# Kernel optimization log

Hardware: AMD Instinct MI355X
Metric: run time of the kernel (lower is better)

Reference implementation:

```python
import jax, jax.numpy as jnp
import numpy as np

B, H, N = 128, 512, 1024

def setup_inputs() -> dict:
    key = jax.random.key(0)
    ks = jax.random.split(key, 9)
    s = 1.0 / np.sqrt(H)
    return {
        "mc_hidden": jax.random.normal(ks[0], (B, H), jnp.float32),
        "sn_hidden": jax.random.normal(ks[1], (B, H, N), jnp.float32),
        "attn_W": jax.random.normal(ks[2], (H, 2 * H), jnp.float32) * s,
        "attn_v": jax.random.normal(ks[3], (H,), jnp.float32) * s,
        "ptr_v": jax.random.normal(ks[4], (H,), jnp.float32) * s,
        "fc1_W": jax.random.normal(ks[5], (H, 2 * H), jnp.float32) * s,
        "fc1_b": jax.random.normal(ks[6], (H,), jnp.float32) * s,
        "fc2_W": jax.random.normal(ks[7], (H, H), jnp.float32) * s,
        "fc2_b": jax.random.normal(ks[8], (H,), jnp.float32) * s,
    }


def reference(mc_hidden, sn_hidden, attn_W, attn_v, ptr_v, fc1_W, fc1_b, fc2_W, fc2_b):
    # ---- Attention (Bahdanau-style additive scoring) ----
    # hidden: (B, 2H, N) = cat(sn_hidden, mc expanded along N) on dim 1
    mc_exp = jnp.broadcast_to(mc_hidden[:, :, None], sn_hidden.shape)  # (B,H,N)
    hidden = jnp.concatenate((sn_hidden, mc_exp), axis=1)              # (B,2H,N)
    # W @ hidden -> (B,H,N); v @ tanh(.) -> (B,N)
    scores = jnp.einsum('h,bhn->bn', attn_v,
                        jnp.tanh(jnp.einsum('hk,bkn->bhn', attn_W, hidden)))
    attns = jax.nn.softmax(scores, axis=-1)                            # (B,N)
    # ---- Context + pointer scoring ----
    context = jnp.einsum('bn,bhn->bh', attns, sn_hidden)               # (B,H)
    x = jnp.concatenate((mc_hidden, context), axis=1)                  # (B,2H)
    out = jax.nn.relu(x @ fc1_W.T + fc1_b)                             # (B,H)
    out = jax.nn.relu(out @ fc2_W.T + fc2_b)                           # (B,H)
    probs = jnp.einsum('h,bhn->bn', ptr_v,
                       jnp.tanh(sn_hidden + out[:, :, None]))          # (B,N)
    return probs
```

## Files before the change

kernel.cpp:

```cpp
#include <hip/hip_runtime.h>
#include <hip/hip_bf16.h>

#define Bn 128
#define Hd 512
#define Nn 1024

typedef __attribute__((ext_vector_type(8))) short short8;
typedef __attribute__((ext_vector_type(4))) float f32x4;

#define GLOAD_LDS16(gptr, lptr)                                                     \
    __builtin_amdgcn_global_load_lds(                                               \
        (const __attribute__((address_space(1))) void*)(gptr),                      \
        (__attribute__((address_space(3))) void*)(lptr), 16, 0, 0)

__device__ __forceinline__ float bf2f(unsigned u) {
    unsigned v = u << 16;
    float f;
    __builtin_memcpy(&f, &v, 4);
    return f;
}

__device__ __forceinline__ unsigned short f2bf(float f) {
    unsigned x;
    __builtin_memcpy(&x, &f, 4);
    unsigned r = x + 0x7fffu + ((x >> 16) & 1u);
    return (unsigned short)(r >> 16);
}

__device__ __forceinline__ unsigned pack_bf2(float a, float b) {
    __hip_bfloat162 h = __float22bfloat162_rn(float2{a, b});
    unsigned u;
    __builtin_memcpy(&u, &h, 4);
    return u;
}

__device__ __forceinline__ float wave_sum(float v) {
    v += __shfl_xor(v, 32);
    v += __shfl_xor(v, 16);
    v += __shfl_xor(v, 8);
    v += __shfl_xor(v, 4);
    v += __shfl_xor(v, 2);
    v += __shfl_xor(v, 1);
    return v;
}

__device__ __forceinline__ float tanh_fast(float x) {
    float e = __expf(2.0f * x);
    return 1.0f - 2.0f * __builtin_amdgcn_rcpf(e + 1.0f);
}

__global__ void convert_W_kernel(const float* __restrict__ attn_W,
                                 unsigned short* __restrict__ Wb) {
    int idx = (blockIdx.x * 256 + threadIdx.x) * 8;
    int h = idx >> 9;
    int k = idx & 511;
    const float* p = attn_W + (size_t)h * 1024 + k;
    float4 v0 = *(const float4*)p;
    float4 v1 = *(const float4*)(p + 4);
    unsigned u[4] = {pack_bf2(v0.x, v0.y), pack_bf2(v0.z, v0.w),
                     pack_bf2(v1.x, v1.y), pack_bf2(v1.z, v1.w)};
    *(uint4*)(Wb + idx) = *(uint4*)u;
}

__global__ void transpose_sn_kernel(const float* __restrict__ sn,
                                    unsigned short* __restrict__ snT) {
    __shared__ unsigned ldsb[32 * 132];
    int bid = blockIdx.x;
    int b = bid >> 6;
    int kt = (bid >> 3) & 7;
    int nt = bid & 7;
    int k0 = kt << 6, n0 = nt << 7;
    int t = threadIdx.x;

    int kp_l = t >> 5;
    int n4 = (t & 31) * 4;
#pragma unroll
    for (int j = 0; j < 4; ++j) {
        int kp = j * 8 + kp_l;
        const float* p0 = sn + ((size_t)(b * Hd + k0 + 2 * kp)) * Nn + n0 + n4;
        float4 f0 = *(const float4*)p0;
        float4 f1 = *(const float4*)(p0 + Nn);
        unsigned u[4];
        u[0] = pack_bf2(f0.x, f1.x);
        u[1] = pack_bf2(f0.y, f1.y);
        u[2] = pack_bf2(f0.z, f1.z);
        u[3] = pack_bf2(f0.w, f1.w);
        *(uint4*)&ldsb[kp * 132 + n4] = *(uint4*)u;
    }
    __syncthreads();

    int c = t & 7;
#pragma unroll
    for (int it = 0; it < 4; ++it) {
        int n = (t >> 3) + it * 32;
        unsigned u[4];
#pragma unroll
        for (int i = 0; i < 4; ++i) u[i] = ldsb[(c * 4 + i) * 132 + n];
        unsigned short* dst = snT + ((size_t)(b * Nn) + n0 + n) * Hd + k0 + c * 8;
        *(uint4*)dst = *(uint4*)u;
    }
}

__global__ void mc_term_kernel(const float* __restrict__ mc,
                               const float* __restrict__ attn_W,
                               float* __restrict__ mc_term) {
    int wg = (blockIdx.x * blockDim.x + threadIdx.x) >> 6;
    int lane = threadIdx.x & 63;
    int b = wg >> 9;
    int h = wg & 511;
    const float* m = mc + b * Hd + lane * 8;
    const float* w = attn_W + (size_t)h * 1024 + 512 + lane * 8;
    float4 m0 = *(const float4*)m, m1 = *(const float4*)(m + 4);
    float4 w0 = *(const float4*)w, w1 = *(const float4*)(w + 4);
    float acc = m0.x * w0.x + m0.y * w0.y + m0.z * w0.z + m0.w * w0.w +
                m1.x * w1.x + m1.y * w1.y + m1.z * w1.z + m1.w * w1.w;
    acc = wave_sum(acc);
    if (lane == 0) mc_term[b * Hd + h] = acc;
}

__global__ __launch_bounds__(256, 2)
void attn_score_kernel(const unsigned short* __restrict__ snT,
                       const unsigned short* __restrict__ Wb,
                       const float* __restrict__ attn_v,
                       const float* __restrict__ mc_term,
                       float* __restrict__ scores) {
    __shared__ __align__(16) unsigned short A_lds[256 * 64];
    __shared__ __align__(16) unsigned short B_lds[128 * 64];
    __shared__ float av_s[256];
    __shared__ float mct_s[256];
    __shared__ float ssum[128];

    const int bid = blockIdx.x;
    const int b = bid >> 4;
    const int mh = (bid >> 3) & 1;
    const int n0 = (bid & 7) << 7;
    const int tid = threadIdx.x;
    const int lane = tid & 63;
    const int wid = tid >> 6;
    const int quad = lane >> 4;
    const int l15 = lane & 15;

    av_s[tid] = attn_v[mh * 256 + tid];
    mct_s[tid] = mc_term[b * Hd + mh * 256 + tid];
    if (tid < 128) ssum[tid] = 0.f;

    f32x4 acc[4][8];
#pragma unroll
    for (int i = 0; i < 4; ++i)
#pragma unroll
        for (int j = 0; j < 8; ++j) {
            f32x4 z = {0.f, 0.f, 0.f, 0.f};
            acc[i][j] = z;
        }

    const int r8 = lane >> 3;
    const int csw = ((lane & 7) ^ r8) * 16;
    const char* Wg = (const char*)Wb + (size_t)(mh * 256) * 1024;
    const char* Bg = (const char*)snT + ((size_t)(b * Nn + n0)) * 1024;
    const int key = l15 & 7;

    for (int k0 = 0; k0 < 512; k0 += 64) {
#pragma unroll
        for (int i = 0; i < 8; ++i) {
            const int row = wid * 64 + i * 8;
            GLOAD_LDS16(Wg + (size_t)(row + r8) * 1024 + k0 * 2 + csw,
                        (char*)A_lds + row * 128);
        }
#pragma unroll
        for (int i = 0; i < 4; ++i) {
            const int row = wid * 32 + i * 8;
            GLOAD_LDS16(Bg + (size_t)(row + r8) * 1024 + k0 * 2 + csw,
                        (char*)B_lds + row * 128);
        }
        __syncthreads();
#pragma unroll
        for (int kk = 0; kk < 2; ++kk) {
            const int cb = quad + kk * 4;
            short8 bfr[8], afr[4];
#pragma unroll
            for (int nt = 0; nt < 8; ++nt) {
                const int n = nt * 16 + l15;
                bfr[nt] = *(const short8*)((const char*)B_lds + n * 128 + ((cb ^ key) * 16));
            }
#pragma unroll
            for (int mt = 0; mt < 4; ++mt) {
                const int m = wid * 64 + mt * 16 + l15;
                afr[mt] = *(const short8*)((const char*)A_lds + m * 128 + ((cb ^ key) * 16));
            }
#pragma unroll
            for (int mt = 0; mt < 4; ++mt)
#pragma unroll
                for (int nt = 0; nt < 8; ++nt)
                    acc[mt][nt] = __builtin_amdgcn_mfma_f32_16x16x32_bf16(afr[mt], bfr[nt], acc[mt][nt], 0, 0, 0);
        }
        __syncthreads();
    }

    float s[8] = {0.f, 0.f, 0.f, 0.f, 0.f, 0.f, 0.f, 0.f};
#pragma unroll
    for (int mt = 0; mt < 4; ++mt) {
        int hb = wid * 64 + mt * 16 + quad * 4;
#pragma unroll
        for (int r = 0; r < 4; ++r) {
            float av = av_s[hb + r];
            float mcv = mct_s[hb + r];
#pragma unroll
            for (int nt = 0; nt < 8; ++nt)
                s[nt] += av * tanh_fast(acc[mt][nt][r] + mcv);
        }
    }
#pragma unroll
    for (int nt = 0; nt < 8; ++nt) {
        float v = s[nt];
        v += __shfl_xor(v, 16);
        v += __shfl_xor(v, 32);
        if (lane < 16) atomicAdd(&ssum[nt * 16 + l15], v);
    }
    __syncthreads();
    if (tid < 128) atomicAdd(&scores[b * Nn + n0 + tid], ssum[tid]);
}

__global__ void softmax_context_kernel(const unsigned short* __restrict__ snT,
                                       const float* __restrict__ scores,
                                       float* __restrict__ context) {
    int b = blockIdx.x >> 3;
    int nc = (blockIdx.x & 7) << 7;
    int t = threadIdx.x;
    int lane = t & 63, wid = t >> 6;
    __shared__ float red[4];
    __shared__ float a_s[128];

    float v[4];
#pragma unroll
    for (int i = 0; i < 4; ++i) v[i] = scores[b * Nn + t + i * 256];
    float m = fmaxf(fmaxf(v[0], v[1]), fmaxf(v[2], v[3]));
#pragma unroll
    for (int off = 32; off >= 1; off >>= 1) m = fmaxf(m, __shfl_xor(m, off));
    if (lane == 0) red[wid] = m;
    __syncthreads();
    m = fmaxf(fmaxf(red[0], red[1]), fmaxf(red[2], red[3]));
    __syncthreads();
    float s = 0.f;
#pragma unroll
    for (int i = 0; i < 4; ++i) s += __expf(v[i] - m);
    s = wave_sum(s);
    if (lane == 0) red[wid] = s;
    __syncthreads();
    s = red[0] + red[1] + red[2] + red[3];
    float inv = __builtin_amdgcn_rcpf(s);
    if (t < 128) a_s[t] = __expf(scores[b * Nn + nc + t] - m) * inv;
    __syncthreads();

    const unsigned short* base = snT + ((size_t)(b * Nn) + nc) * Hd + t * 2;
    float acc0 = 0.f, acc1 = 0.f;
#pragma unroll 4
    for (int i = 0; i < 128; ++i) {
        unsigned d = *(const unsigned*)(base + (size_t)i * Hd);
        float a = a_s[i];
        acc0 += a * bf2f(d & 0xffffu);
        acc1 += a * bf2f(d >> 16);
    }
    atomicAdd(&context[b * Hd + 2 * t], acc0);
    atomicAdd(&context[b * Hd + 2 * t + 1], acc1);
}

__global__ void fc1_kernel(const float* __restrict__ mc,
                           const float* __restrict__ ctx,
                           const float* __restrict__ fc1_W,
                           const float* __restrict__ fc1_b,
                           float* __restrict__ out1) {
    int wg = (blockIdx.x * blockDim.x + threadIdx.x) >> 6;
    int lane = threadIdx.x & 63;
    int b = wg >> 9, h = wg & 511;
    const float* wr = fc1_W + (size_t)h * 1024;
    float acc = 0.f;
    {
        float4 w0 = *(const float4*)(wr + lane * 8);
        float4 w1 = *(const float4*)(wr + lane * 8 + 4);
        float4 x0 = *(const float4*)(mc + b * Hd + lane * 8);
        float4 x1 = *(const float4*)(mc + b * Hd + lane * 8 + 4);
        acc += w0.x * x0.x + w0.y * x0.y + w0.z * x0.z + w0.w * x0.w;
        acc += w1.x * x1.x + w1.y * x1.y + w1.z * x1.z + w1.w * x1.w;
    }
    {
        float4 w0 = *(const float4*)(wr + 512 + lane * 8);
        float4 w1 = *(const float4*)(wr + 512 + lane * 8 + 4);
        float4 x0 = *(const float4*)(ctx + b * Hd + lane * 8);
        float4 x1 = *(const float4*)(ctx + b * Hd + lane * 8 + 4);
        acc += w0.x * x0.x + w0.y * x0.y + w0.z * x0.z + w0.w * x0.w;
        acc += w1.x * x1.x + w1.y * x1.y + w1.z * x1.z + w1.w * x1.w;
    }
    acc = wave_sum(acc);
    if (lane == 0) out1[b * Hd + h] = fmaxf(acc + fc1_b[h], 0.f);
}

__global__ void fc2_kernel(const float* __restrict__ out1,
                           const float* __restrict__ fc2_W,
                           const float* __restrict__ fc2_b,
                           float* __restrict__ out2) {
    int wg = (blockIdx.x * blockDim.x + threadIdx.x) >> 6;
    int lane = threadIdx.x & 63;
    int b = wg >> 9, h = wg & 511;
    const float* wr = fc2_W + (size_t)h * 512 + lane * 8;
    float4 w0 = *(const float4*)wr;
    float4 w1 = *(const float4*)(wr + 4);
    float4 x0 = *(const float4*)(out1 + b * Hd + lane * 8);
    float4 x1 = *(const float4*)(out1 + b * Hd + lane * 8 + 4);
    float acc = w0.x * x0.x + w0.y * x0.y + w0.z * x0.z + w0.w * x0.w +
                w1.x * x1.x + w1.y * x1.y + w1.z * x1.z + w1.w * x1.w;
    acc = wave_sum(acc);
    if (lane == 0) out2[b * Hd + h] = fmaxf(acc + fc2_b[h], 0.f);
}

__global__ void final_kernel(const unsigned short* __restrict__ snT,
                             const float* __restrict__ ptr_v,
                             const float* __restrict__ out2,
                             float* __restrict__ probs) {
    int b = blockIdx.x >> 4;
    int n0 = (blockIdx.x & 15) << 6;
    int t = threadIdx.x;
    int n = n0 + (t >> 2), p = t & 3;
    __shared__ float pv_s[512], o2_s[512];
    pv_s[t] = ptr_v[t];
    pv_s[t + 256] = ptr_v[t + 256];
    o2_s[t] = out2[b * Hd + t];
    o2_s[t + 256] = out2[b * Hd + t + 256];
    __syncthreads();
    const unsigned short* row = snT + ((size_t)(b * Nn) + n) * Hd + p * 8;
    float a = 0.f;
#pragma unroll 4
    for (int j = 0; j < 16; ++j) {
        uint4 d = *(const uint4*)(row + j * 32);
        int hb = p * 8 + j * 32;
        const unsigned* u = (const unsigned*)&d;
#pragma unroll
        for (int q = 0; q < 4; ++q) {
            int h = hb + q * 2;
            float x0 = bf2f(u[q] & 0xffffu);
            float x1 = bf2f(u[q] >> 16);
            a += pv_s[h] * tanh_fast(x0 + o2_s[h]);
            a += pv_s[h + 1] * tanh_fast(x1 + o2_s[h + 1]);
        }
    }
    a += __shfl_xor(a, 1);
    a += __shfl_xor(a, 2);
    if (p == 0) probs[b * Nn + n] = a;
}

extern "C" void kernel_launch(void* const* d_in, const int* in_sizes, int n_in,
                              void* d_out, int out_size, void* d_ws, size_t ws_size,
                              hipStream_t stream) {
    const float* mc  = (const float*)d_in[0];
    const float* sn  = (const float*)d_in[1];
    const float* aW  = (const float*)d_in[2];
    const float* av  = (const float*)d_in[3];
    const float* pv  = (const float*)d_in[4];
    const float* f1W = (const float*)d_in[5];
    const float* f1b = (const float*)d_in[6];
    const float* f2W = (const float*)d_in[7];
    const float* f2b = (const float*)d_in[8];

    unsigned short* snT = (unsigned short*)d_ws;
    unsigned short* Wb  = snT + (size_t)Bn * Nn * Hd;
    float* fws     = (float*)(Wb + 512 * 512);
    float* mc_term = fws;
    float* scores  = mc_term + Bn * Hd;
    float* context = scores + Bn * Nn;
    float* out1    = context + Bn * Hd;
    float* out2    = out1 + Bn * Hd;
    float* probs   = (float*)d_out;

    hipMemsetAsync(scores, 0, (Bn * Nn + Bn * Hd) * sizeof(float), stream);
    convert_W_kernel<<<dim3(128), dim3(256), 0, stream>>>(aW, Wb);
    transpose_sn_kernel<<<dim3(8192), dim3(256), 0, stream>>>(sn, snT);
    mc_term_kernel<<<dim3(16384), dim3(256), 0, stream>>>(mc, aW, mc_term);
    attn_score_kernel<<<dim3(2048), dim3(256), 0, stream>>>(snT, Wb, av, mc_term, scores);
    softmax_context_kernel<<<dim3(1024), dim3(256), 0, stream>>>(snT, scores, context);
    fc1_kernel<<<dim3(16384), dim3(256), 0, stream>>>(mc, context, f1W, f1b, out1);
    fc2_kernel<<<dim3(16384), dim3(256), 0, stream>>>(out1, f2W, f2b, out2);
    final_kernel<<<dim3(2048), dim3(256), 0, stream>>>(snT, pv, out2, probs);
}
```

Baseline: 552.7 us.

## Drop sn transpose pass; consume fp32 sn directly in attention, context, final

Removes the separate bf16 transpose of sn_hidden and converts to bf16 on the fly inside the attention MFMA kernel, staging through registers into a k-pair LDS layout. Context and final kernels now read fp32 sn in its native layout with coalesced float4 loads. Softmax is split out, and score atomics are replaced by per-half partial buffers, which removes the memset. The trade is more fp32 bytes read per consumer, with scalar LDS gathers for the B fragments, in exchange for skipping the transpose write and one launch.

```diff
diff --git a/kernel.cpp b/kernel.cpp
--- a/kernel.cpp
+++ b/kernel.cpp
@@ -12,20 +12,6 @@
     __builtin_amdgcn_global_load_lds(                                               \
         (const __attribute__((address_space(1))) void*)(gptr),                      \
         (__attribute__((address_space(3))) void*)(lptr), 16, 0, 0)
-
-__device__ __forceinline__ float bf2f(unsigned u) {
-    unsigned v = u << 16;
-    float f;
-    __builtin_memcpy(&f, &v, 4);
-    return f;
-}
-
-__device__ __forceinline__ unsigned short f2bf(float f) {
-    unsigned x;
-    __builtin_memcpy(&x, &f, 4);
-    unsigned r = x + 0x7fffu + ((x >> 16) & 1u);
-    return (unsigned short)(r >> 16);
-}
 
 __device__ __forceinline__ unsigned pack_bf2(float a, float b) {
     __hip_bfloat162 h = __float22bfloat162_rn(float2{a, b});
@@ -49,62 +35,23 @@
     return 1.0f - 2.0f * __builtin_amdgcn_rcpf(e + 1.0f);
 }
 
-__global__ void convert_W_kernel(const float* __restrict__ attn_W,
-                                 unsigned short* __restrict__ Wb) {
-    int idx = (blockIdx.x * 256 + threadIdx.x) * 8;
-    int h = idx >> 9;
-    int k = idx & 511;
-    const float* p = attn_W + (size_t)h * 1024 + k;
-    float4 v0 = *(const float4*)p;
-    float4 v1 = *(const float4*)(p + 4);
-    unsigned u[4] = {pack_bf2(v0.x, v0.y), pack_bf2(v0.z, v0.w),
-                     pack_bf2(v1.x, v1.y), pack_bf2(v1.z, v1.w)};
-    *(uint4*)(Wb + idx) = *(uint4*)u;
-}
-
-__global__ void transpose_sn_kernel(const float* __restrict__ sn,
-                                    unsigned short* __restrict__ snT) {
-    __shared__ unsigned ldsb[32 * 132];
-    int bid = blockIdx.x;
-    int b = bid >> 6;
-    int kt = (bid >> 3) & 7;
-    int nt = bid & 7;
-    int k0 = kt << 6, n0 = nt << 7;
-    int t = threadIdx.x;
-
-    int kp_l = t >> 5;
-    int n4 = (t & 31) * 4;
-#pragma unroll
-    for (int j = 0; j < 4; ++j) {
-        int kp = j * 8 + kp_l;
-        const float* p0 = sn + ((size_t)(b * Hd + k0 + 2 * kp)) * Nn + n0 + n4;
-        float4 f0 = *(const float4*)p0;
-        float4 f1 = *(const float4*)(p0 + Nn);
-        unsigned u[4];
-        u[0] = pack_bf2(f0.x, f1.x);
-        u[1] = pack_bf2(f0.y, f1.y);
-        u[2] = pack_bf2(f0.z, f1.z);
-        u[3] = pack_bf2(f0.w, f1.w);
-        *(uint4*)&ldsb[kp * 132 + n4] = *(uint4*)u;
-    }
-    __syncthreads();
-
-    int c = t & 7;
-#pragma unroll
-    for (int it = 0; it < 4; ++it) {
-        int n = (t >> 3) + it * 32;
-        unsigned u[4];
-#pragma unroll
-        for (int i = 0; i < 4; ++i) u[i] = ldsb[(c * 4 + i) * 132 + n];
-        unsigned short* dst = snT + ((size_t)(b * Nn) + n0 + n) * Hd + k0 + c * 8;
-        *(uint4*)dst = *(uint4*)u;
-    }
-}
-
-__global__ void mc_term_kernel(const float* __restrict__ mc,
-                               const float* __restrict__ attn_W,
-                               float* __restrict__ mc_term) {
-    int wg = (blockIdx.x * blockDim.x + threadIdx.x) >> 6;
+__global__ void pre_kernel(const float* __restrict__ attn_W,
+                           const float* __restrict__ mc,
+                           unsigned short* __restrict__ Wb,
+                           float* __restrict__ mc_term) {
+    if (blockIdx.x < 128) {
+        int idx = (blockIdx.x * 256 + threadIdx.x) * 8;
+        int h = idx >> 9;
+        int k = idx & 511;
+        const float* p = attn_W + (size_t)h * 1024 + k;
+        float4 v0 = *(const float4*)p;
+        float4 v1 = *(const float4*)(p + 4);
+        unsigned u[4] = {pack_bf2(v0.x, v0.y), pack_bf2(v0.z, v0.w),
+                         pack_bf2(v1.x, v1.y), pack_bf2(v1.z, v1.w)};
+        *(uint4*)(Wb + idx) = *(uint4*)u;
+        return;
+    }
+    int wg = ((blockIdx.x - 128) * 256 + threadIdx.x) >> 6;
     int lane = threadIdx.x & 63;
     int b = wg >> 9;
     int h = wg & 511;
@@ -119,13 +66,13 @@
 }
 
 __global__ __launch_bounds__(256, 2)
-void attn_score_kernel(const unsigned short* __restrict__ snT,
+void attn_score_kernel(const float* __restrict__ sn,
                        const unsigned short* __restrict__ Wb,
                        const float* __restrict__ attn_v,
                        const float* __restrict__ mc_term,
-                       float* __restrict__ scores) {
+                       float* __restrict__ scores_part) {
     __shared__ __align__(16) unsigned short A_lds[256 * 64];
-    __shared__ __align__(16) unsigned short B_lds[128 * 64];
+    __shared__ __align__(16) unsigned B_kp[32 * 132];
     __shared__ float av_s[256];
     __shared__ float mct_s[256];
     __shared__ float ssum[128];
@@ -156,8 +103,11 @@
     const int r8 = lane >> 3;
     const int csw = ((lane & 7) ^ r8) * 16;
     const char* Wg = (const char*)Wb + (size_t)(mh * 256) * 1024;
-    const char* Bg = (const char*)snT + ((size_t)(b * Nn + n0)) * 1024;
     const int key = l15 & 7;
+
+    const int kp_l = tid >> 5;
+    const int n4 = (tid & 31) * 4;
+    const float* snb = sn + (size_t)b * Hd * Nn + n0 + n4;
 
     for (int k0 = 0; k0 < 512; k0 += 64) {
 #pragma unroll
@@ -167,10 +117,17 @@
                         (char*)A_lds + row * 128);
         }
 #pragma unroll
-        for (int i = 0; i < 4; ++i) {
-            const int row = wid * 32 + i * 8;
-            GLOAD_LDS16(Bg + (size_t)(row + r8) * 1024 + k0 * 2 + csw,
-                        (char*)B_lds + row * 128);
+        for (int j = 0; j < 4; ++j) {
+            const int kp = j * 8 + kp_l;
+            const float* p0 = snb + (size_t)(k0 + 2 * kp) * Nn;
+            float4 f0 = *(const float4*)p0;
+            float4 f1 = *(const float4*)(p0 + Nn);
+            unsigned u[4];
+            u[0] = pack_bf2(f0.x, f1.x);
+            u[1] = pack_bf2(f0.y, f1.y);
+            u[2] = pack_bf2(f0.z, f1.z);
+            u[3] = pack_bf2(f0.w, f1.w);
+            *(uint4*)&B_kp[kp * 132 + n4] = *(uint4*)u;
         }
         __syncthreads();
 #pragma unroll
@@ -179,8 +136,13 @@
             short8 bfr[8], afr[4];
 #pragma unroll
             for (int nt = 0; nt < 8; ++nt) {
-                const int n = nt * 16 + l15;
-                bfr[nt] = *(const short8*)((const char*)B_lds + n * 128 + ((cb ^ key) * 16));
+                const int nl = nt * 16 + l15;
+                uint4 uu;
+                uu.x = B_kp[(cb * 4 + 0) * 132 + nl];
+                uu.y = B_kp[(cb * 4 + 1) * 132 + nl];
+                uu.z = B_kp[(cb * 4 + 2) * 132 + nl];
+                uu.w = B_kp[(cb * 4 + 3) * 132 + nl];
+                bfr[nt] = *(short8*)&uu;
             }
 #pragma unroll
             for (int mt = 0; mt < 4; ++mt) {
@@ -217,22 +179,24 @@
         if (lane < 16) atomicAdd(&ssum[nt * 16 + l15], v);
     }
     __syncthreads();
-    if (tid < 128) atomicAdd(&scores[b * Nn + n0 + tid], ssum[tid]);
-}
-
-__global__ void softmax_context_kernel(const unsigned short* __restrict__ snT,
-                                       const float* __restrict__ scores,
-                                       float* __restrict__ context) {
-    int b = blockIdx.x >> 3;
-    int nc = (blockIdx.x & 7) << 7;
-    int t = threadIdx.x;
-    int lane = t & 63, wid = t >> 6;
+    if (tid < 128)
+        scores_part[((size_t)mh * Bn + b) * Nn + n0 + tid] = ssum[tid];
+}
+
+__global__ void softmax_kernel(const float* __restrict__ scores_part,
+                               float* __restrict__ attns) {
+    const int b = blockIdx.x;
+    const int tid = threadIdx.x;
+    const int lane = tid & 63, wid = tid >> 6;
     __shared__ float red[4];
-    __shared__ float a_s[128];
-
+    const float* s0 = scores_part + (size_t)b * Nn;
+    const float* s1 = scores_part + ((size_t)Bn + b) * Nn;
     float v[4];
 #pragma unroll
-    for (int i = 0; i < 4; ++i) v[i] = scores[b * Nn + t + i * 256];
+    for (int i = 0; i < 4; ++i) {
+        int idx = tid + i * 256;
+        v[i] = s0[idx] + s1[idx];
+    }
     float m = fmaxf(fmaxf(v[0], v[1]), fmaxf(v[2], v[3]));
 #pragma unroll
     for (int off = 32; off >= 1; off >>= 1) m = fmaxf(m, __shfl_xor(m, off));
@@ -242,26 +206,41 @@
     __syncthreads();
     float s = 0.f;
 #pragma unroll
-    for (int i = 0; i < 4; ++i) s += __expf(v[i] - m);
+    for (int i = 0; i < 4; ++i) {
+        v[i] = __expf(v[i] - m);
+        s += v[i];
+    }
     s = wave_sum(s);
     if (lane == 0) red[wid] = s;
     __syncthreads();
     s = red[0] + red[1] + red[2] + red[3];
     float inv = __builtin_amdgcn_rcpf(s);
-    if (t < 128) a_s[t] = __expf(scores[b * Nn + nc + t] - m) * inv;
-    __syncthreads();
-
-    const unsigned short* base = snT + ((size_t)(b * Nn) + nc) * Hd + t * 2;
-    float acc0 = 0.f, acc1 = 0.f;
-#pragma unroll 4
-    for (int i = 0; i < 128; ++i) {
-        unsigned d = *(const unsigned*)(base + (size_t)i * Hd);
-        float a = a_s[i];
-        acc0 += a * bf2f(d & 0xffffu);
-        acc1 += a * bf2f(d >> 16);
-    }
-    atomicAdd(&context[b * Hd + 2 * t], acc0);
-    atomicAdd(&context[b * Hd + 2 * t + 1], acc1);
+#pragma unroll
+    for (int i = 0; i < 4; ++i) attns[b * Nn + tid + i * 256] = v[i] * inv;
+}
+
+__global__ void context_kernel(const float* __restrict__ sn,
+                               const float* __restrict__ attns,
+                               float* __restrict__ context) {
+    int b = blockIdx.x >> 3;
+    int h0 = (blockIdx.x & 7) << 6;
+    int t = threadIdx.x;
+    __shared__ float a_s[1024];
+    *(float4*)&a_s[t * 4] = *(const float4*)&attns[b * Nn + t * 4];
+    __syncthreads();
+    int h = h0 + (t >> 2), q = t & 3;
+    const float* row = sn + ((size_t)b * Hd + h) * Nn;
+    float acc = 0.f;
+#pragma unroll 8
+    for (int j = 0; j < 64; ++j) {
+        int n = q * 4 + j * 16;
+        float4 f = *(const float4*)&row[n];
+        float4 a = *(const float4*)&a_s[n];
+        acc += f.x * a.x + f.y * a.y + f.z * a.z + f.w * a.w;
+    }
+    acc += __shfl_xor(acc, 1);
+    acc += __shfl_xor(acc, 2);
+    if (q == 0) context[b * Hd + h] = acc;
 }
 
 __global__ void fc1_kernel(const float* __restrict__ mc,
@@ -312,39 +291,40 @@
     if (lane == 0) out2[b * Hd + h] = fmaxf(acc + fc2_b[h], 0.f);
 }
 
-__global__ void final_kernel(const unsigned short* __restrict__ snT,
+__global__ void final_kernel(const float* __restrict__ sn,
                              const float* __restrict__ ptr_v,
                              const float* __restrict__ out2,
                              float* __restrict__ probs) {
-    int b = blockIdx.x >> 4;
-    int n0 = (blockIdx.x & 15) << 6;
+    int b = blockIdx.x >> 2;
+    int n0 = (blockIdx.x & 3) << 8;
     int t = threadIdx.x;
-    int n = n0 + (t >> 2), p = t & 3;
+    int w = t >> 6, l = t & 63;
     __shared__ float pv_s[512], o2_s[512];
+    __shared__ float fsum[4][256];
     pv_s[t] = ptr_v[t];
     pv_s[t + 256] = ptr_v[t + 256];
     o2_s[t] = out2[b * Hd + t];
     o2_s[t + 256] = out2[b * Hd + t + 256];
     __syncthreads();
-    const unsigned short* row = snT + ((size_t)(b * Nn) + n) * Hd + p * 8;
-    float a = 0.f;
+    const float* col = sn + (size_t)b * Hd * Nn + n0 + l * 4;
+    float a0 = 0.f, a1 = 0.f, a2 = 0.f, a3 = 0.f;
 #pragma unroll 4
-    for (int j = 0; j < 16; ++j) {
-        uint4 d = *(const uint4*)(row + j * 32);
-        int hb = p * 8 + j * 32;
-        const unsigned* u = (const unsigned*)&d;
-#pragma unroll
-        for (int q = 0; q < 4; ++q) {
-            int h = hb + q * 2;
-            float x0 = bf2f(u[q] & 0xffffu);
-            float x1 = bf2f(u[q] >> 16);
-            a += pv_s[h] * tanh_fast(x0 + o2_s[h]);
-            a += pv_s[h + 1] * tanh_fast(x1 + o2_s[h + 1]);
-        }
-    }
-    a += __shfl_xor(a, 1);
-    a += __shfl_xor(a, 2);
-    if (p == 0) probs[b * Nn + n] = a;
+    for (int j = 0; j < 128; ++j) {
+        int h = w * 128 + j;
+        float4 f = *(const float4*)&col[(size_t)h * Nn];
+        float p = pv_s[h], o = o2_s[h];
+        a0 += p * tanh_fast(f.x + o);
+        a1 += p * tanh_fast(f.y + o);
+        a2 += p * tanh_fast(f.z + o);
+        a3 += p * tanh_fast(f.w + o);
+    }
+    fsum[w][l * 4 + 0] = a0;
+    fsum[w][l * 4 + 1] = a1;
+    fsum[w][l * 4 + 2] = a2;
+    fsum[w][l * 4 + 3] = a3;
+    __syncthreads();
+    float r = fsum[0][t & 255] + fsum[1][t & 255] + fsum[2][t & 255] + fsum[3][t & 255];
+    probs[b * Nn + n0 + (t & 255)] = r;
 }
 
 extern "C" void kernel_launch(void* const* d_in, const int* in_sizes, int n_in,
@@ -360,23 +340,21 @@
     const float* f2W = (const float*)d_in[7];
     const float* f2b = (const float*)d_in[8];
 
-    unsigned short* snT = (unsigned short*)d_ws;
-    unsigned short* Wb  = snT + (size_t)Bn * Nn * Hd;
-    float* fws     = (float*)(Wb + 512 * 512);
-    float* mc_term = fws;
-    float* scores  = mc_term + Bn * Hd;
-    float* context = scores + Bn * Nn;
-    float* out1    = context + Bn * Hd;
-    float* out2    = out1 + Bn * Hd;
-    float* probs   = (float*)d_out;
-
-    hipMemsetAsync(scores, 0, (Bn * Nn + Bn * Hd) * sizeof(float), stream);
-    convert_W_kernel<<<dim3(128), dim3(256), 0, stream>>>(aW, Wb);
-    transpose_sn_kernel<<<dim3(8192), dim3(256), 0, stream>>>(sn, snT);
-    mc_term_kernel<<<dim3(16384), dim3(256), 0, stream>>>(mc, aW, mc_term);
-    attn_score_kernel<<<dim3(2048), dim3(256), 0, stream>>>(snT, Wb, av, mc_term, scores);
-    softmax_context_kernel<<<dim3(1024), dim3(256), 0, stream>>>(snT, scores, context);
+    unsigned short* Wb = (unsigned short*)d_ws;
+    float* fws         = (float*)(Wb + 512 * 512);
+    float* mc_term     = fws;
+    float* scores_part = mc_term + Bn * Hd;
+    float* attns       = scores_part + 2 * Bn * Nn;
+    float* context     = attns + Bn * Nn;
+    float* out1        = context + Bn * Hd;
+    float* out2        = out1 + Bn * Hd;
+    float* probs       = (float*)d_out;
+
+    pre_kernel<<<dim3(16512), dim3(256), 0, stream>>>(aW, mc, Wb, mc_term);
+    attn_score_kernel<<<dim3(2048), dim3(256), 0, stream>>>(sn, Wb, av, mc_term, scores_part);
+    softmax_kernel<<<dim3(128), dim3(256), 0, stream>>>(scores_part, attns);
+    context_kernel<<<dim3(1024), dim3(256), 0, stream>>>(sn, attns, context);
     fc1_kernel<<<dim3(16384), dim3(256), 0, stream>>>(mc, context, f1W, f1b, out1);
     fc2_kernel<<<dim3(16384), dim3(256), 0, stream>>>(out1, f2W, f2b, out2);
-    final_kernel<<<dim3(2048), dim3(256), 0, stream>>>(snT, pv, out2, probs);
-}
+    final_kernel<<<dim3(512), dim3(256), 0, stream>>>(sn, pv, out2, probs);
+}
```

New measurement: 527.3 us. -4.6%, faster.
